# Performance work log

Measured on AMD Instinct MI355X. Metric: run time of the kernel, lower is better.

## Reference

```python
import jax, jax.numpy as jnp
import numpy as np

D_MODEL = 768
N_HEADS = 12
D_K = D_MODEL // N_HEADS


def setup_inputs() -> dict:
    key = jax.random.key(0)
    kq, kk, kv, kwq, kbq, kwo, kbo = jax.random.split(key, 7)
    B, S = 1, 4096
    s = 1.0 / np.sqrt(D_MODEL)
    return {
        "q": jax.random.normal(kq, (B, S, D_MODEL), jnp.float32),
        "k": jax.random.normal(kk, (B, S, D_MODEL), jnp.float32),
        "v": jax.random.normal(kv, (B, S, D_MODEL), jnp.float32),
        # nn.Linear weights stored as [out, in]; note the original forward
        # uses W_q for Q, K, AND V (W_k/W_v are never used), so only W_q and
        # W_o are materialized here.
        "Wq": jax.random.uniform(kwq, (D_MODEL, D_MODEL), jnp.float32, -s, s),
        "bq": jax.random.uniform(kbq, (D_MODEL,), jnp.float32, -s, s),
        "Wo": jax.random.uniform(kwo, (D_MODEL, D_MODEL), jnp.float32, -s, s),
        "bo": jax.random.uniform(kbo, (D_MODEL,), jnp.float32, -s, s),
    }


def _split_heads(x):  # [B,S,D] -> [B,H,S,Dk]
    B, S, _ = x.shape
    return x.reshape(B, S, N_HEADS, D_K).transpose(0, 2, 1, 3)


def reference(q, k, v, Wq, bq, Wo, bo):
    # Faithful to source: same W_q projection applied to q, k, v.
    Q = _split_heads(q @ Wq.T + bq)
    K = _split_heads(k @ Wq.T + bq)
    V = _split_heads(v @ Wq.T + bq)
    scale = 1.0 / np.sqrt(D_K).astype(np.float32)
    scores = jnp.einsum("bhqd,bhkd->bhqk", Q, K) * scale  # [B,H,S,S]
    probs = jax.nn.softmax(scores, axis=-1)
    atten = jnp.einsum("bhqk,bhkd->bhqd", probs, V)
    B, _, S, _ = atten.shape
    concat = atten.transpose(0, 2, 1, 3).reshape(B, S, D_MODEL)
    return concat @ Wo.T + bo
```

## Files before the change

kernel.cpp:

```cpp
#include <hip/hip_runtime.h>
#include <stdint.h>
#include <math.h>


#define SQ 4096
#define DM 768
#define NH 12

typedef float f32x4 __attribute__((ext_vector_type(4)));
typedef short bf16x8 __attribute__((ext_vector_type(8)));
typedef unsigned int u32x4 __attribute__((ext_vector_type(4)));
typedef unsigned short ushort_t;

static __device__ __forceinline__ ushort_t f2bf(float f) {
    unsigned int u = __builtin_bit_cast(unsigned int, f);
    u += 0x7fffu + ((u >> 16) & 1u);
    return (ushort_t)(u >> 16);
}

static __device__ __forceinline__ unsigned int cvt_pk_bf16(float a, float b) {
    unsigned int d;
    asm("v_cvt_pk_bf16_f32 %0, %1, %2" : "=v"(d) : "v"(a), "v"(b));
    return d;
}

static __device__ __forceinline__ void gload16(const ushort_t* g, ushort_t* l) {
    __builtin_amdgcn_global_load_lds(
        reinterpret_cast<const __attribute__((address_space(1))) unsigned int*>(
            reinterpret_cast<uintptr_t>(g)),
        reinterpret_cast<__attribute__((address_space(3))) unsigned int*>(
            reinterpret_cast<uintptr_t>(l)),
        16, 0, 0);
}

__global__ __launch_bounds__(256) void cvt_all(
    const float* __restrict__ q, const float* __restrict__ k,
    const float* __restrict__ v, const float* __restrict__ Wq,
    const float* __restrict__ Wo, ushort_t* __restrict__ xb,
    ushort_t* __restrict__ wqb, ushort_t* __restrict__ wob) {
    const int NE4 = (SQ * DM) / 4;
    const int NW4 = (DM * DM) / 4;
    int i = blockIdx.x * 256 + threadIdx.x;
    const float* src;
    ushort_t* dst;
    if (i < NE4) { src = q; dst = xb; }
    else if (i < 2 * NE4) { src = k; dst = xb + SQ * DM; i -= NE4; }
    else if (i < 3 * NE4) { src = v; dst = xb + 2 * SQ * DM; i -= 2 * NE4; }
    else if (i < 3 * NE4 + NW4) { src = Wq; dst = wqb; i -= 3 * NE4; }
    else if (i < 3 * NE4 + 2 * NW4) { src = Wo; dst = wob; i -= 3 * NE4 + NW4; }
    else return;
    float4 x = reinterpret_cast<const float4*>(src)[i];
    ushort4 o;
    o.x = f2bf(x.x); o.y = f2bf(x.y); o.z = f2bf(x.z); o.w = f2bf(x.w);
    reinterpret_cast<ushort4*>(dst)[i] = o;
}

template <int EPI>
__global__ __launch_bounds__(256) void gemm_bf16(
    const ushort_t* __restrict__ A, const ushort_t* __restrict__ B,
    const float* __restrict__ bias, ushort_t* __restrict__ proj,
    ushort_t* __restrict__ vt, float* __restrict__ outf) {
    __shared__ __align__(16) ushort_t lsA[128 * 64];
    __shared__ __align__(16) ushort_t lsB[128 * 64];
    const int tid = threadIdx.x;
    const int lane = tid & 63;
    const int w = tid >> 6;
    const int wm = w >> 1, wn = w & 1;
    const int g = lane >> 4, li = lane & 15;
    const int bm = blockIdx.x / 6, bn = blockIdx.x % 6;
    const int arow = bm * 128, brow = bn * 128;
    const int sr = lane >> 3;
    const int sc = ((lane & 7) ^ sr) * 8;

    f32x4 acc[4][4] = {};

    for (int kt = 0; kt < 12; ++kt) {
        const int k0 = kt * 64;
        __syncthreads();
#pragma unroll
        for (int c = 0; c < 4; ++c) {
            const int chunk = w * 4 + c;
            const int r = chunk * 8 + sr;
            gload16(A + (size_t)(arow + r) * DM + k0 + sc, lsA + chunk * 512);
            gload16(B + (size_t)(brow + r) * DM + k0 + sc, lsB + chunk * 512);
        }
        __syncthreads();

        bf16x8 af[4][2];
#pragma unroll
        for (int mf = 0; mf < 4; ++mf) {
            const int row = wm * 64 + mf * 16 + li;
#pragma unroll
            for (int ks = 0; ks < 2; ++ks)
                af[mf][ks] = *reinterpret_cast<const bf16x8*>(
                    lsA + row * 64 + ((ks * 32 + g * 8) ^ ((li & 7) << 3)));
        }
#pragma unroll
        for (int nf = 0; nf < 4; ++nf) {
            const int row = wn * 64 + nf * 16 + li;
            bf16x8 b0 = *reinterpret_cast<const bf16x8*>(
                lsB + row * 64 + ((g * 8) ^ ((li & 7) << 3)));
            bf16x8 b1 = *reinterpret_cast<const bf16x8*>(
                lsB + row * 64 + ((32 + g * 8) ^ ((li & 7) << 3)));
#pragma unroll
            for (int mf = 0; mf < 4; ++mf) {
                acc[mf][nf] = __builtin_amdgcn_mfma_f32_16x16x32_bf16(af[mf][0], b0, acc[mf][nf], 0, 0, 0);
                acc[mf][nf] = __builtin_amdgcn_mfma_f32_16x16x32_bf16(af[mf][1], b1, acc[mf][nf], 0, 0, 0);
            }
        }
    }

    if (EPI == 0) {
        const bool isV = (arow >= 8192);
        const float qscale = (arow < 4096) ? 0.18033688011112042f : 1.0f;
#pragma unroll
        for (int nf = 0; nf < 4; ++nf) {
            const int col = brow + wn * 64 + nf * 16 + li;
            const float bv = bias[col];
#pragma unroll
            for (int mf = 0; mf < 4; ++mf) {
                const int row0 = arow + wm * 64 + mf * 16 + g * 4;
                if (!isV) {
#pragma unroll
                    for (int r = 0; r < 4; ++r)
                        proj[(size_t)(row0 + r) * DM + col] = f2bf((acc[mf][nf][r] + bv) * qscale);
                } else {
                    ushort4 pk;
                    pk.x = f2bf(acc[mf][nf][0] + bv);
                    pk.y = f2bf(acc[mf][nf][1] + bv);
                    pk.z = f2bf(acc[mf][nf][2] + bv);
                    pk.w = f2bf(acc[mf][nf][3] + bv);
                    const int kv = row0 - 8192;
                    const int pos = (kv & ~31) | ((kv & 0xC) << 1) | (((kv >> 4) & 1) << 2);
                    *reinterpret_cast<ushort4*>(vt + (size_t)col * SQ + pos) = pk;
                }
            }
        }
    } else {
#pragma unroll
        for (int nf = 0; nf < 4; ++nf) {
            const int col = brow + wn * 64 + nf * 16 + li;
            const float bv = bias[col];
#pragma unroll
            for (int mf = 0; mf < 4; ++mf) {
                const int row0 = arow + wm * 64 + mf * 16 + g * 4;
#pragma unroll
                for (int r = 0; r < 4; ++r)
                    outf[(size_t)(row0 + r) * DM + col] = acc[mf][nf][r] + bv;
            }
        }
    }
}

__global__ __launch_bounds__(256) void attn_bf16(
    const ushort_t* __restrict__ qk, const ushort_t* __restrict__ vtb,
    ushort_t* __restrict__ cc) {
    __shared__ __align__(16) ushort_t kl[2][64 * 64];
    __shared__ __align__(16) ushort_t vl[2][64 * 64];

    const int tid = threadIdx.x, lane = tid & 63, w = tid >> 6;
    const int g = lane >> 4, li = lane & 15;
    const int logical = (blockIdx.x & 7) * 96 + (blockIdx.x >> 3);
    const int h = logical >> 6, qb = logical & 63;
    const int sr = lane >> 3;
    const int sc = ((lane & 7) ^ sr) * 8;

    const ushort_t* Kb = qk + (size_t)4096 * DM + (size_t)h * 64;
    const ushort_t* Vb = vtb + (size_t)(h * 64) * SQ;

    bf16x8 qf[2];
#pragma unroll
    for (int ks = 0; ks < 2; ++ks)
        qf[ks] = *reinterpret_cast<const bf16x8*>(
            qk + (size_t)(qb * 64 + w * 16 + li) * DM + h * 64 + ks * 32 + g * 8);

    f32x4 oacc[4] = {};
    float lsum = 0.f;

#pragma unroll
    for (int c = 0; c < 2; ++c) {
        const int ch = w * 2 + c;
        const int r = ch * 8 + sr;
        gload16(Kb + (size_t)r * DM + sc, &kl[0][ch * 512]);
        gload16(Vb + (size_t)r * SQ + sc, &vl[0][ch * 512]);
    }
    __syncthreads();

    int cur = 0;
    for (int kv = 0; kv < 64; ++kv) {
        if (kv < 63) {
            const int kvn = (kv + 1) * 64;
#pragma unroll
            for (int c = 0; c < 2; ++c) {
                const int ch = w * 2 + c;
                const int r = ch * 8 + sr;
                gload16(Kb + (size_t)(kvn + r) * DM + sc, &kl[cur ^ 1][ch * 512]);
                gload16(Vb + (size_t)r * SQ + kvn + sc, &vl[cur ^ 1][ch * 512]);
            }
        }
        const ushort_t* kp = kl[cur];
        const ushort_t* vp = vl[cur];

        f32x4 sf[4] = {};
        __builtin_amdgcn_s_setprio(1);
#pragma unroll
        for (int nf = 0; nf < 4; ++nf) {
            const int row = nf * 16 + li;
            bf16x8 kb0 = *reinterpret_cast<const bf16x8*>(
                kp + row * 64 + ((g * 8) ^ ((li & 7) << 3)));
            bf16x8 kb1 = *reinterpret_cast<const bf16x8*>(
                kp + row * 64 + ((32 + g * 8) ^ ((li & 7) << 3)));
            sf[nf] = __builtin_amdgcn_mfma_f32_16x16x32_bf16(kb0, qf[0], sf[nf], 0, 0, 0);
            sf[nf] = __builtin_amdgcn_mfma_f32_16x16x32_bf16(kb1, qf[1], sf[nf], 0, 0, 0);
        }
        __builtin_amdgcn_s_setprio(0);

#pragma unroll
        for (int nf = 0; nf < 4; ++nf) {
            f32x4 p;
#pragma unroll
            for (int r = 0; r < 4; ++r) p[r] = exp2f(sf[nf][r]);
            sf[nf] = p;
            lsum += (p[0] + p[1]) + (p[2] + p[3]);
        }

        __builtin_amdgcn_s_setprio(1);
#pragma unroll
        for (int ks = 0; ks < 2; ++ks) {
            u32x4 pu;
            pu.x = cvt_pk_bf16(sf[2 * ks][0], sf[2 * ks][1]);
            pu.y = cvt_pk_bf16(sf[2 * ks][2], sf[2 * ks][3]);
            pu.z = cvt_pk_bf16(sf[2 * ks + 1][0], sf[2 * ks + 1][1]);
            pu.w = cvt_pk_bf16(sf[2 * ks + 1][2], sf[2 * ks + 1][3]);
            const bf16x8 pa = __builtin_bit_cast(bf16x8, pu);
#pragma unroll
            for (int nv = 0; nv < 4; ++nv) {
                const int vrow = nv * 16 + li;
                bf16x8 vb = *reinterpret_cast<const bf16x8*>(
                    vp + vrow * 64 + ((ks * 32 + g * 8) ^ ((li & 7) << 3)));
                oacc[nv] = __builtin_amdgcn_mfma_f32_16x16x32_bf16(pa, vb, oacc[nv], 0, 0, 0);
            }
        }
        __builtin_amdgcn_s_setprio(0);

        __syncthreads();
        cur ^= 1;
    }

    float s = lsum;
    s += __shfl_xor(s, 16);
    s += __shfl_xor(s, 32);
    float inv[4];
    const int gbase = g << 2;
#pragma unroll
    for (int r = 0; r < 4; ++r)
        inv[r] = 1.0f / __shfl(s, gbase + r);

#pragma unroll
    for (int nv = 0; nv < 4; ++nv)
#pragma unroll
        for (int r = 0; r < 4; ++r) {
            const int row = qb * 64 + w * 16 + g * 4 + r;
            const int col = h * 64 + nv * 16 + li;
            cc[(size_t)row * DM + col] = f2bf(oacc[nv][r] * inv[r]);
        }
}

extern "C" void kernel_launch(void* const* d_in, const int* in_sizes, int n_in,
                              void* d_out, int out_size, void* d_ws, size_t ws_size,
                              hipStream_t stream) {
    const float* q = (const float*)d_in[0];
    const float* k = (const float*)d_in[1];
    const float* v = (const float*)d_in[2];
    const float* Wq = (const float*)d_in[3];
    const float* bq = (const float*)d_in[4];
    const float* Wo = (const float*)d_in[5];
    const float* bo = (const float*)d_in[6];
    float* out = (float*)d_out;

    ushort_t* ws = (ushort_t*)d_ws;
    const int NE = SQ * DM;
    ushort_t* xb = ws;
    ushort_t* wqb = ws + 3 * NE;
    ushort_t* wob = wqb + DM * DM;
    ushort_t* proj = wob + DM * DM;
    ushort_t* vt = proj + 2 * NE;
    ushort_t* cc = vt + NE;

    const int n4 = 3 * (NE / 4) + 2 * ((DM * DM) / 4);
    cvt_all<<<(n4 + 255) / 256, 256, 0, stream>>>(q, k, v, Wq, Wo, xb, wqb, wob);

    gemm_bf16<0><<<(12288 / 128) * 6, 256, 0, stream>>>(xb, wqb, bq, proj, vt, (float*)nullptr);

    attn_bf16<<<NH * (SQ / 64), 256, 0, stream>>>(proj, vt, cc);

    gemm_bf16<1><<<(SQ / 128) * 6, 256, 0, stream>>>(cc, wob, bo, (ushort_t*)nullptr, (ushort_t*)nullptr, out);
}
```

Baseline: 161.0 us.

## Process two query subtiles per wave in attention with 128-thread blocks

The attention kernel now runs 2 waves per block, each handling 32 query rows as two 16-row subtiles, so each K/V fragment read from LDS feeds two MFMAs. The double-buffer loop is manually unrolled by two so buffer pointers are compile-time, and exp2f is replaced by the raw v_exp_f32 instruction. The aim is fewer LDS reads per MFMA and less loop and exp overhead. The cost is higher register pressure and fewer waves per block to hide latency.

```diff
diff --git a/kernel.cpp b/kernel.cpp
--- a/kernel.cpp
+++ b/kernel.cpp
@@ -22,6 +22,12 @@
     unsigned int d;
     asm("v_cvt_pk_bf16_f32 %0, %1, %2" : "=v"(d) : "v"(a), "v"(b));
     return d;
+}
+
+static __device__ __forceinline__ float exp2_hw(float x) {
+    float r;
+    asm("v_exp_f32 %0, %1" : "=v"(r) : "v"(x));
+    return r;
 }
 
 static __device__ __forceinline__ void gload16(const ushort_t* g, ushort_t* l) {
@@ -152,7 +158,7 @@
     }
 }
 
-__global__ __launch_bounds__(256) void attn_bf16(
+__global__ __launch_bounds__(128) void attn_bf16(
     const ushort_t* __restrict__ qk, const ushort_t* __restrict__ vtb,
     ushort_t* __restrict__ cc) {
     __shared__ __align__(16) ushort_t kl[2][64 * 64];
@@ -168,102 +174,113 @@
     const ushort_t* Kb = qk + (size_t)4096 * DM + (size_t)h * 64;
     const ushort_t* Vb = vtb + (size_t)(h * 64) * SQ;
 
-    bf16x8 qf[2];
-#pragma unroll
-    for (int ks = 0; ks < 2; ++ks)
-        qf[ks] = *reinterpret_cast<const bf16x8*>(
-            qk + (size_t)(qb * 64 + w * 16 + li) * DM + h * 64 + ks * 32 + g * 8);
-
-    f32x4 oacc[4] = {};
-    float lsum = 0.f;
-
-#pragma unroll
-    for (int c = 0; c < 2; ++c) {
-        const int ch = w * 2 + c;
+    bf16x8 qf[2][2];
+#pragma unroll
+    for (int qh = 0; qh < 2; ++qh)
+#pragma unroll
+        for (int ks = 0; ks < 2; ++ks)
+            qf[qh][ks] = *reinterpret_cast<const bf16x8*>(
+                qk + (size_t)(qb * 64 + w * 32 + qh * 16 + li) * DM + h * 64 + ks * 32 + g * 8);
+
+    f32x4 oacc[2][4] = {};
+    float lsum0 = 0.f, lsum1 = 0.f;
+
+#pragma unroll
+    for (int c = 0; c < 4; ++c) {
+        const int ch = w * 4 + c;
         const int r = ch * 8 + sr;
         gload16(Kb + (size_t)r * DM + sc, &kl[0][ch * 512]);
         gload16(Vb + (size_t)r * SQ + sc, &vl[0][ch * 512]);
     }
     __syncthreads();
 
-    int cur = 0;
-    for (int kv = 0; kv < 64; ++kv) {
-        if (kv < 63) {
-            const int kvn = (kv + 1) * 64;
-#pragma unroll
-            for (int c = 0; c < 2; ++c) {
-                const int ch = w * 2 + c;
-                const int r = ch * 8 + sr;
-                gload16(Kb + (size_t)(kvn + r) * DM + sc, &kl[cur ^ 1][ch * 512]);
-                gload16(Vb + (size_t)r * SQ + kvn + sc, &vl[cur ^ 1][ch * 512]);
+#define STEP(kp, vp, kn, vn, kvn)                                              \
+    do {                                                                       \
+        if ((kvn) < 64) {                                                      \
+            const int kvo = (kvn) * 64;                                        \
+            _Pragma("unroll") for (int c = 0; c < 4; ++c) {                    \
+                const int ch = w * 4 + c;                                      \
+                const int r = ch * 8 + sr;                                     \
+                gload16(Kb + (size_t)(kvo + r) * DM + sc, &(kn)[ch * 512]);    \
+                gload16(Vb + (size_t)r * SQ + kvo + sc, &(vn)[ch * 512]);      \
+            }                                                                  \
+        }                                                                      \
+        f32x4 sf[2][4] = {};                                                   \
+        __builtin_amdgcn_s_setprio(1);                                         \
+        _Pragma("unroll") for (int nf = 0; nf < 4; ++nf) {                     \
+            const int row = nf * 16 + li;                                      \
+            bf16x8 kb0 = *reinterpret_cast<const bf16x8*>(                     \
+                (kp) + row * 64 + ((g * 8) ^ ((li & 7) << 3)));                \
+            bf16x8 kb1 = *reinterpret_cast<const bf16x8*>(                     \
+                (kp) + row * 64 + ((32 + g * 8) ^ ((li & 7) << 3)));           \
+            _Pragma("unroll") for (int qh = 0; qh < 2; ++qh) {                 \
+                sf[qh][nf] = __builtin_amdgcn_mfma_f32_16x16x32_bf16(          \
+                    kb0, qf[qh][0], sf[qh][nf], 0, 0, 0);                      \
+                sf[qh][nf] = __builtin_amdgcn_mfma_f32_16x16x32_bf16(          \
+                    kb1, qf[qh][1], sf[qh][nf], 0, 0, 0);                      \
+            }                                                                  \
+        }                                                                      \
+        __builtin_amdgcn_s_setprio(0);                                         \
+        _Pragma("unroll") for (int qh = 0; qh < 2; ++qh)                       \
+            _Pragma("unroll") for (int nf = 0; nf < 4; ++nf) {                 \
+                f32x4 p;                                                       \
+                _Pragma("unroll") for (int r = 0; r < 4; ++r)                  \
+                    p[r] = exp2_hw(sf[qh][nf][r]);                             \
+                sf[qh][nf] = p;                                                \
+                const float ps = (p[0] + p[1]) + (p[2] + p[3]);                \
+                if (qh == 0) lsum0 += ps; else lsum1 += ps;                    \
+            }                                                                  \
+        __builtin_amdgcn_s_setprio(1);                                         \
+        _Pragma("unroll") for (int ks = 0; ks < 2; ++ks) {                     \
+            bf16x8 pa[2];                                                      \
+            _Pragma("unroll") for (int qh = 0; qh < 2; ++qh) {                 \
+                u32x4 pu;                                                      \
+                pu.x = cvt_pk_bf16(sf[qh][2 * ks][0], sf[qh][2 * ks][1]);      \
+                pu.y = cvt_pk_bf16(sf[qh][2 * ks][2], sf[qh][2 * ks][3]);      \
+                pu.z = cvt_pk_bf16(sf[qh][2 * ks + 1][0], sf[qh][2 * ks + 1][1]); \
+                pu.w = cvt_pk_bf16(sf[qh][2 * ks + 1][2], sf[qh][2 * ks + 1][3]); \
+                pa[qh] = __builtin_bit_cast(bf16x8, pu);                       \
+            }                                                                  \
+            _Pragma("unroll") for (int nv = 0; nv < 4; ++nv) {                 \
+                const int vrow = nv * 16 + li;                                 \
+                bf16x8 vb = *reinterpret_cast<const bf16x8*>(                  \
+                    (vp) + vrow * 64 + ((ks * 32 + g * 8) ^ ((li & 7) << 3))); \
+                oacc[0][nv] = __builtin_amdgcn_mfma_f32_16x16x32_bf16(         \
+                    pa[0], vb, oacc[0][nv], 0, 0, 0);                          \
+                oacc[1][nv] = __builtin_amdgcn_mfma_f32_16x16x32_bf16(         \
+                    pa[1], vb, oacc[1][nv], 0, 0, 0);                          \
+            }                                                                  \
+        }                                                                      \
+        __builtin_amdgcn_s_setprio(0);                                         \
+        __syncthreads();                                                       \
+    } while (0)
+
+#pragma unroll 1
+    for (int t = 0; t < 32; ++t) {
+        STEP(&kl[0][0], &vl[0][0], &kl[1][0], &vl[1][0], 2 * t + 1);
+        STEP(&kl[1][0], &vl[1][0], &kl[0][0], &vl[0][0], 2 * t + 2);
+    }
+#undef STEP
+
+#pragma unroll
+    for (int qh = 0; qh < 2; ++qh) {
+        float s = (qh == 0) ? lsum0 : lsum1;
+        s += __shfl_xor(s, 16);
+        s += __shfl_xor(s, 32);
+        float inv[4];
+        const int gbase = g << 2;
+#pragma unroll
+        for (int r = 0; r < 4; ++r)
+            inv[r] = 1.0f / __shfl(s, gbase + r);
+#pragma unroll
+        for (int nv = 0; nv < 4; ++nv)
+#pragma unroll
+            for (int r = 0; r < 4; ++r) {
+                const int row = qb * 64 + w * 32 + qh * 16 + g * 4 + r;
+                const int col = h * 64 + nv * 16 + li;
+                cc[(size_t)row * DM + col] = f2bf(oacc[qh][nv][r] * inv[r]);
             }
-        }
-        const ushort_t* kp = kl[cur];
-        const ushort_t* vp = vl[cur];
-
-        f32x4 sf[4] = {};
-        __builtin_amdgcn_s_setprio(1);
-#pragma unroll
-        for (int nf = 0; nf < 4; ++nf) {
-            const int row = nf * 16 + li;
-            bf16x8 kb0 = *reinterpret_cast<const bf16x8*>(
-                kp + row * 64 + ((g * 8) ^ ((li & 7) << 3)));
-            bf16x8 kb1 = *reinterpret_cast<const bf16x8*>(
-                kp + row * 64 + ((32 + g * 8) ^ ((li & 7) << 3)));
-            sf[nf] = __builtin_amdgcn_mfma_f32_16x16x32_bf16(kb0, qf[0], sf[nf], 0, 0, 0);
-            sf[nf] = __builtin_amdgcn_mfma_f32_16x16x32_bf16(kb1, qf[1], sf[nf], 0, 0, 0);
-        }
-        __builtin_amdgcn_s_setprio(0);
-
-#pragma unroll
-        for (int nf = 0; nf < 4; ++nf) {
-            f32x4 p;
-#pragma unroll
-            for (int r = 0; r < 4; ++r) p[r] = exp2f(sf[nf][r]);
-            sf[nf] = p;
-            lsum += (p[0] + p[1]) + (p[2] + p[3]);
-        }
-
-        __builtin_amdgcn_s_setprio(1);
-#pragma unroll
-        for (int ks = 0; ks < 2; ++ks) {
-            u32x4 pu;
-            pu.x = cvt_pk_bf16(sf[2 * ks][0], sf[2 * ks][1]);
-            pu.y = cvt_pk_bf16(sf[2 * ks][2], sf[2 * ks][3]);
-            pu.z = cvt_pk_bf16(sf[2 * ks + 1][0], sf[2 * ks + 1][1]);
-            pu.w = cvt_pk_bf16(sf[2 * ks + 1][2], sf[2 * ks + 1][3]);
-            const bf16x8 pa = __builtin_bit_cast(bf16x8, pu);
-#pragma unroll
-            for (int nv = 0; nv < 4; ++nv) {
-                const int vrow = nv * 16 + li;
-                bf16x8 vb = *reinterpret_cast<const bf16x8*>(
-                    vp + vrow * 64 + ((ks * 32 + g * 8) ^ ((li & 7) << 3)));
-                oacc[nv] = __builtin_amdgcn_mfma_f32_16x16x32_bf16(pa, vb, oacc[nv], 0, 0, 0);
-            }
-        }
-        __builtin_amdgcn_s_setprio(0);
-
-        __syncthreads();
-        cur ^= 1;
-    }
-
-    float s = lsum;
-    s += __shfl_xor(s, 16);
-    s += __shfl_xor(s, 32);
-    float inv[4];
-    const int gbase = g << 2;
-#pragma unroll
-    for (int r = 0; r < 4; ++r)
-        inv[r] = 1.0f / __shfl(s, gbase + r);
-
-#pragma unroll
-    for (int nv = 0; nv < 4; ++nv)
-#pragma unroll
-        for (int r = 0; r < 4; ++r) {
-            const int row = qb * 64 + w * 16 + g * 4 + r;
-            const int col = h * 64 + nv * 16 + li;
-            cc[(size_t)row * DM + col] = f2bf(oacc[nv][r] * inv[r]);
-        }
+    }
 }
 
 extern "C" void kernel_launch(void* const* d_in, const int* in_sizes, int n_in,
@@ -292,7 +309,7 @@
 
     gemm_bf16<0><<<(12288 / 128) * 6, 256, 0, stream>>>(xb, wqb, bq, proj, vt, (float*)nullptr);
 
-    attn_bf16<<<NH * (SQ / 64), 256, 0, stream>>>(proj, vt, cc);
+    attn_bf16<<<NH * (SQ / 64), 128, 0, stream>>>(proj, vt, cc);
 
     gemm_bf16<1><<<(SQ / 128) * 6, 256, 0, stream>>>(cc, wob, bo, (ushort_t*)nullptr, (ushort_t*)nullptr, out);
 }
```

Result: faster. 147.1 us (-8.6%).
